# Kernel optimization log

Measured on AMD Instinct MI355X. Metric: run time of the kernel, lower is better.

The kernel has to match this reference:

```python
import jax, jax.numpy as jnp
import numpy as np

# bitsandbytes NF4 codebook (16 levels)
NF4 = jnp.array([-1.0, -0.6961928009986877, -0.5250730514526367, -0.39491748809814453,
                 -0.28444138169288635, -0.18477343022823334, -0.09105003625154495, 0.0,
                 0.07958029955625534, 0.16093020141124725, 0.24611230194568634,
                 0.33791524171829224, 0.44070982933044434, 0.5626170039176941,
                 0.7229568362236023, 1.0], dtype=jnp.float32)
BLOCK = 64  # NF4 quantization blocksize
HD, M, TOKENS = 4096, 11008, 512


def dequant_nf4(codes, absmax, out_f, in_f):
    # codes: int [out_f, in_f] in [0,16); absmax: float [out_f*in_f/BLOCK]
    w = NF4[codes.reshape(-1, BLOCK)] * absmax[:, None]
    return w.reshape(out_f, in_f)


def setup_inputs() -> dict:
    key = jax.random.key(0)
    ks = jax.random.split(key, 7)
    x = jax.random.normal(ks[0], (TOKENS, HD), dtype=jnp.float32)
    gate_codes = jax.random.randint(ks[1], (M, HD), 0, 16, dtype=jnp.int32)
    up_codes = jax.random.randint(ks[2], (M, HD), 0, 16, dtype=jnp.int32)
    down_codes = jax.random.randint(ks[3], (HD, M), 0, 16, dtype=jnp.int32)
    n_blk = (M * HD) // BLOCK
    gate_absmax = jax.random.uniform(ks[4], (n_blk,), dtype=jnp.float32) * 0.02 + 1e-3
    up_absmax = jax.random.uniform(ks[5], (n_blk,), dtype=jnp.float32) * 0.02 + 1e-3
    down_absmax = jax.random.uniform(ks[6], (n_blk,), dtype=jnp.float32) * 0.02 + 1e-3
    return {"x": x, "gate_codes": gate_codes, "gate_absmax": gate_absmax,
            "up_codes": up_codes, "up_absmax": up_absmax,
            "down_codes": down_codes, "down_absmax": down_absmax}


def reference(x, gate_codes, gate_absmax, up_codes, up_absmax, down_codes, down_absmax):
    # Dequantize NF4 weights on the fly, then SwiGLU MLP:
    # down( silu(gate(x)) * up(x) )
    Wg = dequant_nf4(gate_codes, gate_absmax, M, HD)   # [m, hd]
    Wu = dequant_nf4(up_codes, up_absmax, M, HD)       # [m, hd]
    Wd = dequant_nf4(down_codes, down_absmax, HD, M)   # [hd, m]
    g = x @ Wg.T                                       # [tokens, m]
    u = x @ Wu.T                                       # [tokens, m]
    h = jax.nn.silu(g) * u                             # [tokens, m]
    return h @ Wd.T                                    # [tokens, hd]
```

## Files before the change

kernel.cpp:

```cpp
#include <hip/hip_runtime.h>
#include <hip/hip_fp16.h>
#include <cstdint>
#include <cstddef>


using float4v = __attribute__((ext_vector_type(4))) float;
using half8   = __attribute__((ext_vector_type(8))) _Float16;

__constant__ float NF4TAB[16] = {
  -1.0f, -0.6961928009986877f, -0.5250730514526367f, -0.39491748809814453f,
  -0.28444138169288635f, -0.18477343022823334f, -0.09105003625154495f, 0.0f,
  0.07958029955625534f, 0.16093020141124725f, 0.24611230194568634f,
  0.33791524171829224f, 0.44070982933044434f, 0.5626170039176941f,
  0.7229568362236023f, 1.0f };


__global__ __launch_bounds__(256) void repack_kernel(
    const int* __restrict__ codes, const float* __restrict__ amax,
    unsigned char* __restrict__ pb, float* __restrict__ pam,
    int K, int Kb, int KbG)
{
  const int tid  = threadIdx.x;
  const int lane = tid & 63;
  const int w    = tid >> 6;
  const int l15  = lane & 15;
  const int hi   = lane >> 4;

  const int tile = blockIdx.x / KbG;
  const int kbg  = blockIdx.x % KbG;
  const int kb   = kbg * 4 + w;

  unsigned dk0[4], dk1[4];
  #pragma unroll
  for (int j = 0; j < 4; ++j) {
    const int* base = codes + (size_t)(tile * 64 + j * 16 + l15) * K
                            + (size_t)kb * 64;
    const int4 a0 = *(const int4*)(base + hi * 8);
    const int4 a1 = *(const int4*)(base + hi * 8 + 4);
    const int4 b0 = *(const int4*)(base + 32 + hi * 8);
    const int4 b1 = *(const int4*)(base + 32 + hi * 8 + 4);
    dk0[j] = (unsigned)((a0.x | (a0.y << 4)) | ((a0.z | (a0.w << 4)) << 8) |
                        ((a1.x | (a1.y << 4)) << 16) | ((a1.z | (a1.w << 4)) << 24));
    dk1[j] = (unsigned)((b0.x | (b0.y << 4)) | ((b0.z | (b0.w << 4)) << 8) |
                        ((b1.x | (b1.y << 4)) << 16) | ((b1.z | (b1.w << 4)) << 24));
  }
  uint4 o0, o1;
  o0.x = dk0[0]; o0.y = dk1[0]; o0.z = dk0[1]; o0.w = dk1[1];
  o1.x = dk0[2]; o1.y = dk1[2]; o1.z = dk0[3]; o1.w = dk1[3];
  uint4* dst = (uint4*)(pb + (((size_t)tile * Kb + kb) * 64 + lane) * 32);
  dst[0] = o0; dst[1] = o1;

  if (w == 0) {
    const float4 am = *(const float4*)(amax + (size_t)(tile * 64 + lane) * Kb
                                            + kbg * 4);
    pam[((size_t)tile * Kb + kbg * 4 + 0) * 64 + lane] = am.x;
    pam[((size_t)tile * Kb + kbg * 4 + 1) * 64 + lane] = am.y;
    pam[((size_t)tile * Kb + kbg * 4 + 2) * 64 + lane] = am.z;
    pam[((size_t)tile * Kb + kbg * 4 + 3) * 64 + lane] = am.w;
  }
}

template <bool ATOMIC>
__global__ __launch_bounds__(256, 3) void gemm_nf4(
    const __half* __restrict__ Apk,
    const unsigned char* __restrict__ p0, const float* __restrict__ am0,
    const unsigned char* __restrict__ p1, const float* __restrict__ am1,
    __half* __restrict__ o0, __half* __restrict__ o1,
    float* __restrict__ outF,
    int N, int K, int Kc, int Ntiles)
{
  __shared__ unsigned ptab[256];

  const int tid  = threadIdx.x;
  const int lane = tid & 63;
  const int wave = tid >> 6;
  const int l15  = lane & 15;

  {
    __half2 pr = __floats2half2_rn(NF4TAB[tid & 15], NF4TAB[tid >> 4]);
    ptab[tid] = *(const unsigned*)&pr;
  }
  __syncthreads();

  int nt, r2, mt;
  if (ATOMIC) {
    const int xcd  = blockIdx.x & 7;
    const int slot = blockIdx.x >> 3;
    r2 = xcd >> 1;
    mt = slot & 1;
    nt = (slot >> 1) + (xcd & 1) * 32;
  } else {
    const int nwg = gridDim.x;
    const int bid = (blockIdx.x & 7) * (nwg >> 3) + (blockIdx.x >> 3);
    mt = bid & 1;
    const int r = bid >> 1;
    nt = r % Ntiles;
    r2 = r / Ntiles;
  }

  const int k0 = ATOMIC ? r2 * Kc : 0;
  const int nk = Kc >> 6;
  const unsigned char* pk = (!ATOMIC && r2) ? p1 : p0;
  const float* amx        = (!ATOMIC && r2) ? am1 : am0;
  __half* outH            = (!ATOMIC && r2) ? o1 : o0;

  const int col0 = nt * 64;
  const int Kb   = K >> 6;
  const int kb0q = k0 >> 6;

  const uint4* pc  = (const uint4*)(pk + (((size_t)nt * Kb + kb0q) * 64 + lane) * 32);
  const float* pam = amx + ((size_t)nt * Kb + kb0q) * 64 + l15;

  const int mb0 = mt * 16 + wave * 4;
  const __half* pA = Apk + ((size_t)((k0 >> 5) * 32 + mb0) * 512)
                         + (size_t)lane * 8;

  float4v acc[4][4];
  {
    float4v z = {0.f, 0.f, 0.f, 0.f};
    #pragma unroll
    for (int i = 0; i < 4; ++i)
      #pragma unroll
      for (int j = 0; j < 4; ++j) acc[i][j] = z;
  }

  uint4 q0_0, q1_0, q0_1, q1_1;
  float af_0[4], af_1[4];

#define LOADCQ0(KT)                                                             \
  { const uint4* _p = pc + (size_t)(KT) * 128;                                  \
    q0_0 = _p[0]; q1_0 = _p[1];                                                 \
    const float* _a = pam + (size_t)(KT) * 64;                                  \
    af_0[0] = _a[0]; af_0[1] = _a[16]; af_0[2] = _a[32]; af_0[3] = _a[48]; }
#define LOADCQ1(KT)                                                             \
  { const uint4* _p = pc + (size_t)(KT) * 128;                                  \
    q0_1 = _p[0]; q1_1 = _p[1];                                                 \
    const float* _a = pam + (size_t)(KT) * 64;                                  \
    af_1[0] = _a[0]; af_1[1] = _a[16]; af_1[2] = _a[32]; af_1[3] = _a[48]; }

#define DEQD(DST, D, AM2)                                                       \
  { unsigned _w0 = ptab[(D) & 255];                                             \
    unsigned _w1 = ptab[((D) >> 8) & 255];                                      \
    unsigned _w2 = ptab[((D) >> 16) & 255];                                     \
    unsigned _w3 = ptab[(D) >> 24];                                             \
    __half2 _p0 = __hmul2(*(const __half2*)&_w0, AM2);                          \
    __half2 _p1 = __hmul2(*(const __half2*)&_w1, AM2);                          \
    __half2 _p2 = __hmul2(*(const __half2*)&_w2, AM2);                          \
    __half2 _p3 = __hmul2(*(const __half2*)&_w3, AM2);                          \
    uint4 _wv;                                                                  \
    _wv.x = *(const unsigned*)&_p0; _wv.y = *(const unsigned*)&_p1;             \
    _wv.z = *(const unsigned*)&_p2; _wv.w = *(const unsigned*)&_p3;             \
    DST = *(const half8*)&_wv; }

#define BODY(KT, S)                                                             \
  { half8 bq[4], ap[4];                                                         \
    { const __half _a0 = __float2half(af_##S[0]);                               \
      const __half _a1 = __float2half(af_##S[1]);                               \
      const __half _a2 = __float2half(af_##S[2]);                               \
      const __half _a3 = __float2half(af_##S[3]);                               \
      const __half2 _m0{_a0,_a0}, _m1{_a1,_a1}, _m2{_a2,_a2}, _m3{_a3,_a3};     \
      DEQD(bq[0], q0_##S.x, _m0); DEQD(bq[1], q0_##S.z, _m1);                   \
      DEQD(bq[2], q1_##S.x, _m2); DEQD(bq[3], q1_##S.z, _m3);                   \
      _Pragma("unroll")                                                         \
      for (int _i = 0; _i < 4; ++_i)                                            \
        ap[_i] = *(const half8*)(pA + (size_t)(KT) * 32768 + _i * 512);         \
      _Pragma("unroll")                                                         \
      for (int _i = 0; _i < 4; ++_i)                                            \
        _Pragma("unroll")                                                       \
        for (int _j = 0; _j < 4; ++_j)                                          \
          acc[_i][_j] = __builtin_amdgcn_mfma_f32_16x16x32_f16(ap[_i], bq[_j], acc[_i][_j], 0, 0, 0); \
      DEQD(bq[0], q0_##S.y, _m0); DEQD(bq[1], q0_##S.w, _m1);                   \
      DEQD(bq[2], q1_##S.y, _m2); DEQD(bq[3], q1_##S.w, _m3);                   \
      _Pragma("unroll")                                                         \
      for (int _i = 0; _i < 4; ++_i)                                            \
        ap[_i] = *(const half8*)(pA + (size_t)(KT) * 32768 + 16384 + _i * 512); \
      _Pragma("unroll")                                                         \
      for (int _i = 0; _i < 4; ++_i)                                            \
        _Pragma("unroll")                                                       \
        for (int _j = 0; _j < 4; ++_j)                                          \
          acc[_i][_j] = __builtin_amdgcn_mfma_f32_16x16x32_f16(ap[_i], bq[_j], acc[_i][_j], 0, 0, 0); \
    }                                                                           \
    if ((KT) + 2 < nk) { LOADCQ##S((KT) + 2); } }

  LOADCQ0(0);
  if (nk > 1) LOADCQ1(1);

  int kt = 0;
  while (kt + 2 <= nk) { BODY(kt, 0); BODY(kt + 1, 1); kt += 2; }
  if (kt < nk) BODY(kt, 0);

  if (ATOMIC) {
    const int ccol0 = col0 + l15;
    const int crow0 = mt * 256 + wave * 64 + ((lane >> 4) << 2);
    #pragma unroll
    for (int i = 0; i < 4; ++i)
      #pragma unroll
      for (int j = 0; j < 4; ++j)
        #pragma unroll
        for (int rr = 0; rr < 4; ++rr) {
          const size_t idx = (size_t)(crow0 + i * 16 + rr) * N + (ccol0 + j * 16);
          atomicAdd(&outF[idx], acc[i][j][rr]);
        }
  } else {
    const int jj    = lane & 7;
    const int lb    = (lane >> 3) & 1;
    const int rbase = (lane >> 4) << 2;
    #pragma unroll
    for (int i = 0; i < 4; ++i) {
      const int mb = mb0 + i;
      #pragma unroll
      for (int j = 0; j < 4; ++j) {
        const int kb = nt * 2 + (j >> 1);
        const int lp = ((j & 1) * 2 + lb) * 16 + rbase;
        #pragma unroll
        for (int rr = 0; rr < 4; ++rr) {
          const size_t a = ((size_t)(kb * 32 + mb) * 64 + (lp + rr)) * 8 + jj;
          outH[a] = __float2half(acc[i][j][rr]);
        }
      }
    }
  }
#undef LOADCQ0
#undef LOADCQ1
#undef DEQD
#undef BODY
}

__global__ void cast_pack_kernel(const float* __restrict__ x,
                                 __half* __restrict__ xp, int nGrp) {
  int pid = blockIdx.x * blockDim.x + threadIdx.x;
  if (pid >= nGrp) return;
  const int lane = pid & 63;
  const int grp  = pid >> 6;
  const int mb   = grp & 31;
  const int kb   = grp >> 5;
  const int m = mb * 16 + (lane & 15);
  const int k = kb * 32 + ((lane >> 4) << 3);
  const float4* src = (const float4*)(x + (size_t)m * 4096 + k);
  float4 v0 = src[0], v1 = src[1];
  __half2 h0 = __floats2half2_rn(v0.x, v0.y), h1 = __floats2half2_rn(v0.z, v0.w);
  __half2 h2 = __floats2half2_rn(v1.x, v1.y), h3 = __floats2half2_rn(v1.z, v1.w);
  uint4 o;
  o.x = *(const unsigned*)&h0; o.y = *(const unsigned*)&h1;
  o.z = *(const unsigned*)&h2; o.w = *(const unsigned*)&h3;
  ((uint4*)xp)[pid] = o;
}

__global__ void swiglu_kernel(const __half* __restrict__ g,
                              const __half* __restrict__ u,
                              __half* __restrict__ h, int n2) {
  int i = blockIdx.x * blockDim.x + threadIdx.x;
  if (i < n2) {
    float2 gf = __half22float2(((const __half2*)g)[i]);
    float2 uf = __half22float2(((const __half2*)u)[i]);
    float h0 = gf.x / (1.f + __expf(-gf.x)) * uf.x;
    float h1 = gf.y / (1.f + __expf(-gf.y)) * uf.y;
    ((__half2*)h)[i] = __floats2half2_rn(h0, h1);
  }
}

extern "C" void kernel_launch(void* const* d_in, const int* in_sizes, int n_in,
                              void* d_out, int out_size, void* d_ws, size_t ws_size,
                              hipStream_t stream)
{
  (void)in_sizes; (void)n_in; (void)ws_size;
  const float* x            = (const float*)d_in[0];
  const int*   gate_codes   = (const int*)d_in[1];
  const float* gate_absmax  = (const float*)d_in[2];
  const int*   up_codes     = (const int*)d_in[3];
  const float* up_absmax    = (const float*)d_in[4];
  const int*   down_codes   = (const int*)d_in[5];
  const float* down_absmax  = (const float*)d_in[6];
  float* out = (float*)d_out;

  __half* xp = (__half*)d_ws;
  __half* g  = xp + (size_t)512 * 4096;
  __half* u  = g  + (size_t)512 * 11008;
  unsigned char* pg = (unsigned char*)(u + (size_t)512 * 11008);
  unsigned char* pu = pg + (size_t)172 * 64 * 2048;
  unsigned char* pd = pu + (size_t)172 * 64 * 2048;
  float* amg = (float*)(pd + (size_t)64 * 172 * 2048);
  float* amu = amg + (size_t)172 * 64 * 64;
  float* amd = amu + (size_t)172 * 64 * 64;

  hipMemsetAsync(d_out, 0, (size_t)out_size * sizeof(float), stream);

  cast_pack_kernel<<<1024, 256, 0, stream>>>(x, xp, (512 * 4096) / 8);

  repack_kernel<<<2752, 256, 0, stream>>>(gate_codes, gate_absmax, pg, amg,
                                          4096, 64, 16);
  repack_kernel<<<2752, 256, 0, stream>>>(up_codes, up_absmax, pu, amu,
                                          4096, 64, 16);
  repack_kernel<<<2752, 256, 0, stream>>>(down_codes, down_absmax, pd, amd,
                                          11008, 172, 43);

  gemm_nf4<false><<<688, 256, 0, stream>>>(xp, pg, amg, pu, amu,
                                           g, u, nullptr,
                                           11008, 4096, 4096, 172);

  swiglu_kernel<<<11008, 256, 0, stream>>>(g, u, g, (512 * 11008) / 2);

  gemm_nf4<true><<<512, 256, 0, stream>>>(g, pd, amd,
                                          nullptr, nullptr, nullptr, nullptr,
                                          out, 4096, 11008, 2752, 64);
}
```

Measured before the change: 705.3 us.

## Software-pipeline NF4 dequant ahead of MFMA and stage repack through LDS

The GEMM main loop now dequantizes the first k-half of the next tile into a double-buffered register set while the current tile's MFMAs run, so dequant ALU work overlaps matrix math instead of sitting in front of it. The repack kernel is restructured to read code rows with coalesced int4 loads into a swizzled shared-memory tile, then transpose out of LDS, replacing strided gathers. The price is extra registers for the prefetched B fragments, which could hurt occupancy under the 3-block launch bound. The unconditional LOADCQ1(1) assumes nk>1.

```diff
diff --git a/kernel.cpp b/kernel.cpp
--- a/kernel.cpp
+++ b/kernel.cpp
@@ -18,45 +18,60 @@
 __global__ __launch_bounds__(256) void repack_kernel(
     const int* __restrict__ codes, const float* __restrict__ amax,
     unsigned char* __restrict__ pb, float* __restrict__ pam,
-    int K, int Kb, int KbG)
+    int K, int Kb, int KbW)
 {
+  __shared__ unsigned st[64 * 32];
+  __shared__ float amst[64 * 5];
+
   const int tid  = threadIdx.x;
   const int lane = tid & 63;
   const int w    = tid >> 6;
-  const int l15  = lane & 15;
-  const int hi   = lane >> 4;
-
-  const int tile = blockIdx.x / KbG;
-  const int kbg  = blockIdx.x % KbG;
-  const int kb   = kbg * 4 + w;
-
-  unsigned dk0[4], dk1[4];
-  #pragma unroll
-  for (int j = 0; j < 4; ++j) {
-    const int* base = codes + (size_t)(tile * 64 + j * 16 + l15) * K
-                            + (size_t)kb * 64;
-    const int4 a0 = *(const int4*)(base + hi * 8);
-    const int4 a1 = *(const int4*)(base + hi * 8 + 4);
-    const int4 b0 = *(const int4*)(base + 32 + hi * 8);
-    const int4 b1 = *(const int4*)(base + 32 + hi * 8 + 4);
-    dk0[j] = (unsigned)((a0.x | (a0.y << 4)) | ((a0.z | (a0.w << 4)) << 8) |
-                        ((a1.x | (a1.y << 4)) << 16) | ((a1.z | (a1.w << 4)) << 24));
-    dk1[j] = (unsigned)((b0.x | (b0.y << 4)) | ((b0.z | (b0.w << 4)) << 8) |
-                        ((b1.x | (b1.y << 4)) << 16) | ((b1.z | (b1.w << 4)) << 24));
-  }
-  uint4 o0, o1;
-  o0.x = dk0[0]; o0.y = dk1[0]; o0.z = dk0[1]; o0.w = dk1[1];
-  o1.x = dk0[2]; o1.y = dk1[2]; o1.z = dk0[3]; o1.w = dk1[3];
-  uint4* dst = (uint4*)(pb + (((size_t)tile * Kb + kb) * 64 + lane) * 32);
-  dst[0] = o0; dst[1] = o1;
-
-  if (w == 0) {
-    const float4 am = *(const float4*)(amax + (size_t)(tile * 64 + lane) * Kb
-                                            + kbg * 4);
-    pam[((size_t)tile * Kb + kbg * 4 + 0) * 64 + lane] = am.x;
-    pam[((size_t)tile * Kb + kbg * 4 + 1) * 64 + lane] = am.y;
-    pam[((size_t)tile * Kb + kbg * 4 + 2) * 64 + lane] = am.z;
-    pam[((size_t)tile * Kb + kbg * 4 + 3) * 64 + lane] = am.w;
+
+  const int tile = blockIdx.x / KbW;
+  const int win  = blockIdx.x % KbW;
+
+  {
+    const int* base = codes + (size_t)tile * 64 * K + (size_t)win * 256;
+    const int c0 = lane >> 1;
+    const int hw = lane & 1;
+    #pragma unroll
+    for (int i = 0; i < 16; ++i) {
+      const int row = w * 16 + i;
+      const int4 c = *(const int4*)(base + (size_t)row * K + lane * 4);
+      const unsigned short v =
+        (unsigned short)((c.x | (c.y << 4)) | ((c.z | (c.w << 4)) << 8));
+      const int W = row * 32 + (c0 ^ ((row & 7) << 2));
+      ((unsigned short*)st)[W * 2 + hw] = v;
+    }
+    const int arow = tid >> 2, q = tid & 3;
+    amst[arow * 5 + q] =
+      amax[(size_t)(tile * 64 + arow) * Kb + win * 4 + q];
+  }
+  __syncthreads();
+
+  {
+    const int kbi = tid >> 6;
+    const int l15 = lane & 15;
+    const int hi  = lane >> 4;
+    const int kb  = win * 4 + kbi;
+    unsigned d[4][2];
+    #pragma unroll
+    for (int j = 0; j < 4; ++j) {
+      const int row = j * 16 + l15;
+      const int sw  = (row & 7) << 2;
+      #pragma unroll
+      for (int kk = 0; kk < 2; ++kk) {
+        const int c = kbi * 8 + kk * 4 + hi;
+        d[j][kk] = st[row * 32 + (c ^ sw)];
+      }
+    }
+    uint4 o0, o1;
+    o0.x = d[0][0]; o0.y = d[0][1]; o0.z = d[1][0]; o0.w = d[1][1];
+    o1.x = d[2][0]; o1.y = d[2][1]; o1.z = d[3][0]; o1.w = d[3][1];
+    uint4* dst = (uint4*)(pb + (((size_t)tile * Kb + kb) * 64 + lane) * 32);
+    dst[0] = o0; dst[1] = o1;
+
+    pam[((size_t)tile * Kb + kb) * 64 + lane] = amst[lane * 5 + kbi];
   }
 }
 
@@ -126,6 +141,7 @@
 
   uint4 q0_0, q1_0, q0_1, q1_1;
   float af_0[4], af_1[4];
+  half8 bqk0A[4], bqk0B[4];
 
 #define LOADCQ0(KT)                                                             \
   { const uint4* _p = pc + (size_t)(KT) * 128;                                  \
@@ -152,42 +168,56 @@
     _wv.z = *(const unsigned*)&_p2; _wv.w = *(const unsigned*)&_p3;             \
     DST = *(const half8*)&_wv; }
 
-#define BODY(KT, S)                                                             \
-  { half8 bq[4], ap[4];                                                         \
-    { const __half _a0 = __float2half(af_##S[0]);                               \
-      const __half _a1 = __float2half(af_##S[1]);                               \
-      const __half _a2 = __float2half(af_##S[2]);                               \
-      const __half _a3 = __float2half(af_##S[3]);                               \
-      const __half2 _m0{_a0,_a0}, _m1{_a1,_a1}, _m2{_a2,_a2}, _m3{_a3,_a3};     \
-      DEQD(bq[0], q0_##S.x, _m0); DEQD(bq[1], q0_##S.z, _m1);                   \
-      DEQD(bq[2], q1_##S.x, _m2); DEQD(bq[3], q1_##S.z, _m3);                   \
+#define DEQ4_K0(DST, S)                                                         \
+  { const __half _a0 = __float2half(af_##S[0]);                                 \
+    const __half _a1 = __float2half(af_##S[1]);                                 \
+    const __half _a2 = __float2half(af_##S[2]);                                 \
+    const __half _a3 = __float2half(af_##S[3]);                                 \
+    const __half2 _m0{_a0,_a0}, _m1{_a1,_a1}, _m2{_a2,_a2}, _m3{_a3,_a3};       \
+    DEQD(DST[0], q0_##S.x, _m0); DEQD(DST[1], q0_##S.z, _m1);                   \
+    DEQD(DST[2], q1_##S.x, _m2); DEQD(DST[3], q1_##S.z, _m3); }
+#define DEQ4_K1(DST, S)                                                         \
+  { const __half _a0 = __float2half(af_##S[0]);                                 \
+    const __half _a1 = __float2half(af_##S[1]);                                 \
+    const __half _a2 = __float2half(af_##S[2]);                                 \
+    const __half _a3 = __float2half(af_##S[3]);                                 \
+    const __half2 _m0{_a0,_a0}, _m1{_a1,_a1}, _m2{_a2,_a2}, _m3{_a3,_a3};       \
+    DEQD(DST[0], q0_##S.y, _m0); DEQD(DST[1], q0_##S.w, _m1);                   \
+    DEQD(DST[2], q1_##S.y, _m2); DEQD(DST[3], q1_##S.w, _m3); }
+
+#define BODY(KT, S, SN, CUR, NXT)                                               \
+  { half8 ap[4], bqk1[4];                                                       \
+    _Pragma("unroll")                                                           \
+    for (int _i = 0; _i < 4; ++_i)                                              \
+      ap[_i] = *(const half8*)(pA + (size_t)(KT) * 32768 + _i * 512);           \
+    _Pragma("unroll")                                                           \
+    for (int _i = 0; _i < 4; ++_i)                                              \
       _Pragma("unroll")                                                         \
-      for (int _i = 0; _i < 4; ++_i)                                            \
-        ap[_i] = *(const half8*)(pA + (size_t)(KT) * 32768 + _i * 512);         \
+      for (int _j = 0; _j < 4; ++_j)                                            \
+        acc[_i][_j] = __builtin_amdgcn_mfma_f32_16x16x32_f16(ap[_i], CUR[_j], acc[_i][_j], 0, 0, 0); \
+    DEQ4_K1(bqk1, S);                                                           \
+    _Pragma("unroll")                                                           \
+    for (int _i = 0; _i < 4; ++_i)                                              \
+      ap[_i] = *(const half8*)(pA + (size_t)(KT) * 32768 + 16384 + _i * 512);   \
+    _Pragma("unroll")                                                           \
+    for (int _i = 0; _i < 4; ++_i)                                              \
       _Pragma("unroll")                                                         \
-      for (int _i = 0; _i < 4; ++_i)                                            \
-        _Pragma("unroll")                                                       \
-        for (int _j = 0; _j < 4; ++_j)                                          \
-          acc[_i][_j] = __builtin_amdgcn_mfma_f32_16x16x32_f16(ap[_i], bq[_j], acc[_i][_j], 0, 0, 0); \
-      DEQD(bq[0], q0_##S.y, _m0); DEQD(bq[1], q0_##S.w, _m1);                   \
-      DEQD(bq[2], q1_##S.y, _m2); DEQD(bq[3], q1_##S.w, _m3);                   \
-      _Pragma("unroll")                                                         \
-      for (int _i = 0; _i < 4; ++_i)                                            \
-        ap[_i] = *(const half8*)(pA + (size_t)(KT) * 32768 + 16384 + _i * 512); \
-      _Pragma("unroll")                                                         \
-      for (int _i = 0; _i < 4; ++_i)                                            \
-        _Pragma("unroll")                                                       \
-        for (int _j = 0; _j < 4; ++_j)                                          \
-          acc[_i][_j] = __builtin_amdgcn_mfma_f32_16x16x32_f16(ap[_i], bq[_j], acc[_i][_j], 0, 0, 0); \
-    }                                                                           \
+      for (int _j = 0; _j < 4; ++_j)                                            \
+        acc[_i][_j] = __builtin_amdgcn_mfma_f32_16x16x32_f16(ap[_i], bqk1[_j], acc[_i][_j], 0, 0, 0); \
+    if ((KT) + 1 < nk) { DEQ4_K0(NXT, SN); }                                    \
     if ((KT) + 2 < nk) { LOADCQ##S((KT) + 2); } }
 
   LOADCQ0(0);
-  if (nk > 1) LOADCQ1(1);
+  LOADCQ1(1);
+  DEQ4_K0(bqk0A, 0);
 
   int kt = 0;
-  while (kt + 2 <= nk) { BODY(kt, 0); BODY(kt + 1, 1); kt += 2; }
-  if (kt < nk) BODY(kt, 0);
+  while (kt + 2 <= nk) {
+    BODY(kt,     0, 1, bqk0A, bqk0B);
+    BODY(kt + 1, 1, 0, bqk0B, bqk0A);
+    kt += 2;
+  }
+  if (kt < nk) BODY(kt, 0, 1, bqk0A, bqk0B);
 
   if (ATOMIC) {
     const int ccol0 = col0 + l15;
@@ -223,6 +253,8 @@
 #undef LOADCQ0
 #undef LOADCQ1
 #undef DEQD
+#undef DEQ4_K0
+#undef DEQ4_K1
 #undef BODY
 }
 
```

Result: slower. 791.7 us (+12.3%).

## Fuse three NF4 repack launches and coalesce code reads via swizzled LDS transpose

Applied to the files above, without the earlier changes.

Merges the gate, up and down repack kernels into one launch that picks its matrix from the block index. Each lane now reads contiguous int4 runs along K, packs nibbles into an XOR-swizzled shared-memory tile, and after a barrier each wave reads back the packed words in the layout the GEMM expects. The absmax values are also staged through shared memory. This targets the strided global reads and extra launch overhead of the old repack, at the cost of LDS use and a block-wide sync.

```diff
diff --git a/kernel.cpp b/kernel.cpp
--- a/kernel.cpp
+++ b/kernel.cpp
@@ -16,47 +16,81 @@
 
 
 __global__ __launch_bounds__(256) void repack_kernel(
-    const int* __restrict__ codes, const float* __restrict__ amax,
-    unsigned char* __restrict__ pb, float* __restrict__ pam,
-    int K, int Kb, int KbG)
+    const int* __restrict__ cg, const float* __restrict__ ag,
+    const int* __restrict__ cu, const float* __restrict__ au,
+    const int* __restrict__ cd, const float* __restrict__ ad,
+    unsigned char* __restrict__ pg, float* __restrict__ amg,
+    unsigned char* __restrict__ pu, float* __restrict__ amu,
+    unsigned char* __restrict__ pd, float* __restrict__ amd)
 {
+  __shared__ unsigned st[64 * 32];
+  __shared__ float amst[64 * 5];
+
   const int tid  = threadIdx.x;
   const int lane = tid & 63;
   const int w    = tid >> 6;
-  const int l15  = lane & 15;
-  const int hi   = lane >> 4;
-
-  const int tile = blockIdx.x / KbG;
-  const int kbg  = blockIdx.x % KbG;
-  const int kb   = kbg * 4 + w;
-
-  unsigned dk0[4], dk1[4];
-  #pragma unroll
-  for (int j = 0; j < 4; ++j) {
-    const int* base = codes + (size_t)(tile * 64 + j * 16 + l15) * K
-                            + (size_t)kb * 64;
-    const int4 a0 = *(const int4*)(base + hi * 8);
-    const int4 a1 = *(const int4*)(base + hi * 8 + 4);
-    const int4 b0 = *(const int4*)(base + 32 + hi * 8);
-    const int4 b1 = *(const int4*)(base + 32 + hi * 8 + 4);
-    dk0[j] = (unsigned)((a0.x | (a0.y << 4)) | ((a0.z | (a0.w << 4)) << 8) |
-                        ((a1.x | (a1.y << 4)) << 16) | ((a1.z | (a1.w << 4)) << 24));
-    dk1[j] = (unsigned)((b0.x | (b0.y << 4)) | ((b0.z | (b0.w << 4)) << 8) |
-                        ((b1.x | (b1.y << 4)) << 16) | ((b1.z | (b1.w << 4)) << 24));
-  }
-  uint4 o0, o1;
-  o0.x = dk0[0]; o0.y = dk1[0]; o0.z = dk0[1]; o0.w = dk1[1];
-  o1.x = dk0[2]; o1.y = dk1[2]; o1.z = dk0[3]; o1.w = dk1[3];
-  uint4* dst = (uint4*)(pb + (((size_t)tile * Kb + kb) * 64 + lane) * 32);
-  dst[0] = o0; dst[1] = o1;
-
-  if (w == 0) {
-    const float4 am = *(const float4*)(amax + (size_t)(tile * 64 + lane) * Kb
-                                            + kbg * 4);
-    pam[((size_t)tile * Kb + kbg * 4 + 0) * 64 + lane] = am.x;
-    pam[((size_t)tile * Kb + kbg * 4 + 1) * 64 + lane] = am.y;
-    pam[((size_t)tile * Kb + kbg * 4 + 2) * 64 + lane] = am.z;
-    pam[((size_t)tile * Kb + kbg * 4 + 3) * 64 + lane] = am.w;
+
+  const int bid = blockIdx.x;
+  const int* codes; const float* amax;
+  unsigned char* pb; float* pam;
+  int K, Kb, KbW, rel;
+  if (bid < 2752)      { codes = cg; amax = ag; pb = pg; pam = amg;
+                         K = 4096;  Kb = 64;  KbW = 16; rel = bid; }
+  else if (bid < 5504) { codes = cu; amax = au; pb = pu; pam = amu;
+                         K = 4096;  Kb = 64;  KbW = 16; rel = bid - 2752; }
+  else                 { codes = cd; amax = ad; pb = pd; pam = amd;
+                         K = 11008; Kb = 172; KbW = 43; rel = bid - 5504; }
+  const int tile = rel / KbW;
+  const int win  = rel % KbW;
+
+  {
+    const int* base = codes + (size_t)tile * 64 * K + (size_t)win * 256;
+    int4 c[16];
+    #pragma unroll
+    for (int i = 0; i < 16; ++i) {
+      const int row = w * 16 + i;
+      c[i] = *(const int4*)(base + (size_t)row * K + lane * 4);
+    }
+    const int c0 = lane >> 1;
+    const int hw = lane & 1;
+    #pragma unroll
+    for (int i = 0; i < 16; ++i) {
+      const int row = w * 16 + i;
+      const unsigned short v =
+        (unsigned short)((c[i].x | (c[i].y << 4)) |
+                         ((c[i].z | (c[i].w << 4)) << 8));
+      const int W = row * 32 + (c0 ^ ((row & 7) << 2));
+      ((unsigned short*)st)[W * 2 + hw] = v;
+    }
+    const int arow = tid >> 2, q = tid & 3;
+    amst[arow * 5 + q] =
+      amax[(size_t)(tile * 64 + arow) * Kb + win * 4 + q];
+  }
+  __syncthreads();
+
+  {
+    const int kbi = tid >> 6;
+    const int l15 = lane & 15;
+    const int hi  = lane >> 4;
+    const int kb  = win * 4 + kbi;
+    unsigned d[4][2];
+    #pragma unroll
+    for (int j = 0; j < 4; ++j) {
+      const int row = j * 16 + l15;
+      const int sw  = (row & 7) << 2;
+      #pragma unroll
+      for (int kk = 0; kk < 2; ++kk) {
+        const int c = kbi * 8 + kk * 4 + hi;
+        d[j][kk] = st[row * 32 + (c ^ sw)];
+      }
+    }
+    uint4 o0, o1;
+    o0.x = d[0][0]; o0.y = d[0][1]; o0.z = d[1][0]; o0.w = d[1][1];
+    o1.x = d[2][0]; o1.y = d[2][1]; o1.z = d[3][0]; o1.w = d[3][1];
+    uint4* dst = (uint4*)(pb + (((size_t)tile * Kb + kb) * 64 + lane) * 32);
+    dst[0] = o0; dst[1] = o1;
+
+    pam[((size_t)tile * Kb + kb) * 64 + lane] = amst[lane * 5 + kbi];
   }
 }
 
@@ -287,12 +321,10 @@
 
   cast_pack_kernel<<<1024, 256, 0, stream>>>(x, xp, (512 * 4096) / 8);
 
-  repack_kernel<<<2752, 256, 0, stream>>>(gate_codes, gate_absmax, pg, amg,
-                                          4096, 64, 16);
-  repack_kernel<<<2752, 256, 0, stream>>>(up_codes, up_absmax, pu, amu,
-                                          4096, 64, 16);
-  repack_kernel<<<2752, 256, 0, stream>>>(down_codes, down_absmax, pd, amd,
-                                          11008, 172, 43);
+  repack_kernel<<<8256, 256, 0, stream>>>(gate_codes, gate_absmax,
+                                          up_codes, up_absmax,
+                                          down_codes, down_absmax,
+                                          pg, amg, pu, amu, pd, amd);
 
   gemm_nf4<false><<<688, 256, 0, stream>>>(xp, pg, amg, pu, amu,
                                            g, u, nullptr,
```

Result: no change. 701.7 us (-0.5%).
